# Kernel optimization log

Measured on AMD Instinct MI355X. Metric: run time of the kernel, lower is better.

## Reference

```python
import jax, jax.numpy as jnp
import numpy as np

DIM = 256; D_STATE = 16; D_CONV = 4; EXPAND = 2; NS = 64
D_INNER = EXPAND * DIM; DT_RANK = (DIM + 15) // 16
B_SZ = 2; H = 64; W = 64


def setup_inputs() -> dict:
    key = jax.random.key(0)
    ks = jax.random.split(key, 32)
    g = lambda i, shape, s=0.02: jax.random.normal(ks[i], shape, dtype=jnp.float32) * s
    inp = {}
    inp["x"] = jax.random.normal(ks[0], (B_SZ, DIM, H, W), dtype=jnp.float32)
    inp["ln_w"] = jnp.ones((DIM,), jnp.float32)
    inp["ln_b"] = jnp.zeros((DIM,), jnp.float32)
    inp["in_proj_w"] = g(1, (2 * D_INNER, DIM))
    for suf, base in (("", 2), ("_b", 10), ("_s", 18)):
        inp["conv_w" + suf] = g(base, (D_INNER, D_CONV), 0.1)
        inp["conv_b" + suf] = g(base + 1, (D_INNER,), 0.1)
        inp["x_proj_w" + suf] = g(base + 2, (DT_RANK + 2 * D_STATE, D_INNER))
        inp["dt_proj_w" + suf] = g(base + 3, (D_INNER, DT_RANK), 0.1)
        inp["dt_proj_b" + suf] = g(base + 4, (D_INNER,), 0.5)
        inp["D" + suf] = jnp.ones((D_INNER,), jnp.float32)
    A_log = jnp.tile(jnp.log(jnp.arange(1, D_STATE + 1, dtype=jnp.float32)), (D_INNER, 1))
    inp["A_log"] = A_log
    inp["A_log_b"] = A_log
    inp["A_log_s"] = A_log
    inp["out_proj_w"] = g(26, (DIM, D_INNER))
    return inp


def _silu(x):
    return x * jax.nn.sigmoid(x)


def _causal_conv(x, w, b):
    # x: (B, L, D); w: (D, K) depthwise causal conv along L
    K = w.shape[1]; L = x.shape[1]
    xp = jnp.pad(x, ((0, 0), (K - 1, 0), (0, 0)))
    y = b
    for k in range(K):
        y = y + xp[:, k:k + L, :] * w[:, k]
    return y


def _ssm_dir(x, z, conv_w, conv_b, x_proj_w, dt_proj_w, dt_proj_b, A_log, Dp):
    # one directional Mamba inner fn (no out_proj); x, z: (B, L, d_inner)
    Bsz, L, Din = x.shape
    xc = _silu(_causal_conv(x, conv_w, conv_b))
    x_dbl = xc @ x_proj_w.T  # (B, L, dt_rank + 2*d_state)
    dt_r = x_dbl[..., :DT_RANK]
    Bm = x_dbl[..., DT_RANK:DT_RANK + D_STATE]
    Cm = x_dbl[..., DT_RANK + D_STATE:]
    dt = jax.nn.softplus(dt_r @ dt_proj_w.T + dt_proj_b)  # (B, L, d_inner)
    A = -jnp.exp(A_log)  # (d_inner, d_state)

    def step(h, inp):
        dt_t, x_t, B_t, C_t = inp
        dA = jnp.exp(dt_t[..., None] * A)  # (B, d_inner, d_state)
        h = dA * h + (dt_t * x_t)[..., None] * B_t[:, None, :]
        return h, jnp.einsum('bds,bs->bd', h, C_t)

    h0 = jnp.zeros((Bsz, Din, D_STATE), x.dtype)
    _, ys = jax.lax.scan(step, h0, (dt.transpose(1, 0, 2), xc.transpose(1, 0, 2),
                                    Bm.transpose(1, 0, 2), Cm.transpose(1, 0, 2)))
    y = ys.transpose(1, 0, 2) + xc * Dp
    return y * _silu(z)


def reference(x, ln_w, ln_b, in_proj_w,
              conv_w, conv_b, x_proj_w, dt_proj_w, dt_proj_b, D,
              conv_w_b, conv_b_b, x_proj_w_b, dt_proj_w_b, dt_proj_b_b, D_b,
              conv_w_s, conv_b_s, x_proj_w_s, dt_proj_w_s, dt_proj_b_s, D_s,
              A_log, A_log_b, A_log_s, out_proj_w):
    Bsz, C, Hh, Ww = x.shape
    L = Hh * Ww
    xf = x.reshape(Bsz, C, L).transpose(0, 2, 1)  # (B, L, C)
    mu = xf.mean(-1, keepdims=True)
    var = ((xf - mu) ** 2).mean(-1, keepdims=True)
    xn = (xf - mu) / jnp.sqrt(var + 1e-5) * ln_w + ln_b
    xz = xn @ in_proj_w.T  # (B, L, 2*d_inner), shared across directions
    xin, z = xz[..., :D_INNER], xz[..., D_INNER:]
    # forward scan
    y_f = _ssm_dir(xin, z, conv_w, conv_b, x_proj_w, dt_proj_w, dt_proj_b, A_log, D)
    # backward scan (flip sequence, scan, flip back)
    y_b = _ssm_dir(xin[:, ::-1], z[:, ::-1], conv_w_b, conv_b_b, x_proj_w_b,
                   dt_proj_w_b, dt_proj_b_b, A_log_b, D_b)[:, ::-1]
    # slice-interleaved scan: 'b (s i) d -> b (i s) d' with s = NS slices
    def il(t):
        return t.reshape(Bsz, NS, L // NS, D_INNER).transpose(0, 2, 1, 3).reshape(Bsz, L, D_INNER)
    def dil(t):
        return t.reshape(Bsz, L // NS, NS, D_INNER).transpose(0, 2, 1, 3).reshape(Bsz, L, D_INNER)
    y_s = dil(_ssm_dir(il(xin), il(z), conv_w_s, conv_b_s, x_proj_w_s,
                       dt_proj_w_s, dt_proj_b_s, A_log_s, D_s))
    out = (y_f + y_b + y_s) @ out_proj_w.T  # (B, L, C)
    return x + out.transpose(0, 2, 1).reshape(Bsz, C, Hh, Ww)
```

## Files before the change

kernel.cpp:

```cpp
#include <hip/hip_runtime.h>
#include <hip/hip_bf16.h>
#include <cstdint>

#define B_SZ 2
#define DIM 256
#define L_SEQ 4096
#define D_INNER 512
#define DT_RANK 16
#define D_STATE 16
#define NCHUNK 64
#define CHUNK 64

static constexpr size_t SZ_BIG_SH = (size_t)B_SZ * L_SEQ * D_INNER;

typedef __attribute__((ext_vector_type(8))) short short8v;
typedef __attribute__((ext_vector_type(4))) short short4v;
typedef __attribute__((ext_vector_type(4))) float f32x4;

__device__ __forceinline__ float silu_f(float v) {
    return v / (1.0f + __expf(-v));
}
__device__ __forceinline__ float softplus_fast(float v) {
    return (v > 15.0f) ? v : __logf(1.0f + __expf(v));
}
__device__ __forceinline__ short f2bf(float f) {
    uint32_t u = __float_as_uint(f);
    u += 0x7fffu + ((u >> 16) & 1u);
    return (short)(u >> 16);
}
__device__ __forceinline__ float bf2f(short s) {
    return __uint_as_float(((uint32_t)(uint16_t)s) << 16);
}
__device__ __forceinline__ int dir_map(int p, int dm) {
    if (dm == 0) return p;
    if (dm == 1) return (L_SEQ - 1) - p;
    return ((p & 63) << 6) | (p >> 6);
}
__device__ __forceinline__ void pow_dA(float r1, float* dA) {
    const float r2 = r1 * r1, r4 = r2 * r2, r8 = r4 * r4;
    dA[0] = r1;         dA[1] = r2;         dA[2] = r2 * r1;    dA[3] = r4;
    dA[4] = r4 * r1;    dA[5] = r4 * r2;    dA[6] = r4 * dA[2]; dA[7] = r8;
    dA[8] = r8 * r1;    dA[9] = r8 * r2;    dA[10] = r8 * dA[2]; dA[11] = r8 * r4;
    dA[12] = r8 * dA[4]; dA[13] = r8 * dA[5]; dA[14] = r8 * dA[6]; dA[15] = r8 * r8;
}

__global__ __launch_bounds__(256) void k_cvt(
    const float* __restrict__ Wi, const float* __restrict__ Wo,
    const float* __restrict__ xp0, const float* __restrict__ xp1, const float* __restrict__ xp2,
    const float* __restrict__ dw0, const float* __restrict__ dw1, const float* __restrict__ dw2,
    short* __restrict__ Wib, short* __restrict__ Wob,
    short* __restrict__ xpwb, short* __restrict__ dtwb)
{
    const int idx = blockIdx.x * 256 + threadIdx.x;
    const float* src; short* dst; int off;
    if (idx < 65536)        { src = Wi; dst = Wib; off = idx; }
    else if (idx < 98304)   { src = Wo; dst = Wob; off = idx - 65536; }
    else if (idx < 116736)  {
        int k = idx - 98304; const int d = k / 6144; k -= d * 6144;
        src = d == 0 ? xp0 : (d == 1 ? xp1 : xp2);
        dst = xpwb + (size_t)d * 24576; off = k;
    } else {
        int k = idx - 116736; const int d = k / 2048; k -= d * 2048;
        src = d == 0 ? dw0 : (d == 1 ? dw1 : dw2);
        dst = dtwb + (size_t)d * 8192; off = k;
    }
    const float4 v = *(const float4*)(src + (size_t)off * 4);
    short4v p = {f2bf(v.x), f2bf(v.y), f2bf(v.z), f2bf(v.w)};
    *(short4v*)(dst + (size_t)off * 4) = p;
}

__global__ __launch_bounds__(256) void k_ln_t(
    const float* __restrict__ x, const float* __restrict__ lnw,
    const float* __restrict__ lnb, short* __restrict__ xnb)
{
    __shared__ float xt[64][257];
    __shared__ float red[2][4][64];
    __shared__ float muS[64], rsS[64];
    __shared__ float lnwS[DIM], lnbS[DIM];

    const int b  = blockIdx.x >> 6;
    const int l0 = (blockIdx.x & 63) << 6;
    const int t  = threadIdx.x;
    lnwS[t] = lnw[t]; lnbS[t] = lnb[t];

    const float* xb = x + (size_t)b * DIM * L_SEQ + l0;
#pragma unroll
    for (int it = 0; it < 16; ++it) {
        const int idx = it * 256 + t;
        const int c = idx >> 4, pos = (idx & 15) << 2;
        const float4 v = *(const float4*)(xb + (size_t)c * L_SEQ + pos);
        xt[pos + 0][c] = v.x; xt[pos + 1][c] = v.y;
        xt[pos + 2][c] = v.z; xt[pos + 3][c] = v.w;
    }
    __syncthreads();
    {
        const int l = t & 63, cq = t >> 6;
        float sum = 0.f, sq = 0.f;
        for (int c = cq * 64; c < cq * 64 + 64; ++c) {
            const float v = xt[l][c];
            sum += v; sq += v * v;
        }
        red[0][cq][l] = sum; red[1][cq][l] = sq;
    }
    __syncthreads();
    if (t < 64) {
        const float s  = red[0][0][t] + red[0][1][t] + red[0][2][t] + red[0][3][t];
        const float q2 = red[1][0][t] + red[1][1][t] + red[1][2][t] + red[1][3][t];
        const float mu  = s * (1.0f / DIM);
        const float var = q2 * (1.0f / DIM) - mu * mu;
        muS[t] = mu; rsS[t] = rsqrtf(var + 1e-5f);
    }
    __syncthreads();
#pragma unroll
    for (int it = 0; it < 32; ++it) {
        const int idx = it * 256 + t;
        const int l = idx >> 7, cp = (idx & 127) << 1;
        const float mu = muS[l], rs = rsS[l];
        short2 p;
        p.x = f2bf((xt[l][cp + 0] - mu) * rs * lnwS[cp + 0] + lnbS[cp + 0]);
        p.y = f2bf((xt[l][cp + 1] - mu) * rs * lnwS[cp + 1] + lnbS[cp + 1]);
        *(short2*)(xnb + (size_t)((b * L_SEQ) + l0 + l) * DIM + cp) = p;
    }
}

__global__ __launch_bounds__(256) void k_inproj_mfma(
    const short* __restrict__ xnb, const short* __restrict__ Wib,
    short* __restrict__ xinb, short* __restrict__ szb)
{
    const int mblk = blockIdx.x >> 2;
    const int q    = blockIdx.x & 3;
    const int t = threadIdx.x;
    const int w = t >> 6, l = t & 63;
    const int m0 = mblk * 64 + w * 16;
    const int n0 = q * 256;
    const int lrow = l & 15, lk = l >> 4;

    short8v a[8];
    {
        const short* ap = xnb + (size_t)(m0 + lrow) * DIM + lk * 8;
#pragma unroll
        for (int kk = 0; kk < 8; ++kk)
            a[kk] = *(const short8v*)(ap + kk * 32);
    }

#pragma unroll 4
    for (int nf = 0; nf < 16; ++nf) {
        const int n = n0 + nf * 16 + lrow;
        const short* bp = Wib + (size_t)n * DIM + lk * 8;
        f32x4 acc = {0.f, 0.f, 0.f, 0.f};
#pragma unroll
        for (int kk = 0; kk < 8; ++kk)
            acc = __builtin_amdgcn_mfma_f32_16x16x32_bf16(
                a[kk], *(const short8v*)(bp + kk * 32), acc, 0, 0, 0);
        const int col = n;
        const int r0  = m0 + lk * 4;
        if (n0 < D_INNER) {
#pragma unroll
            for (int j = 0; j < 4; ++j)
                xinb[(size_t)(r0 + j) * D_INNER + col] = f2bf(acc[j]);
        } else {
#pragma unroll
            for (int j = 0; j < 4; ++j)
                szb[(size_t)(r0 + j) * D_INNER + (col - D_INNER)] = f2bf(silu_f(acc[j]));
        }
    }
}

__global__ __launch_bounds__(256) void k_conv3(
    const short* __restrict__ xinb,
    const float* __restrict__ cw0, const float* __restrict__ cw1, const float* __restrict__ cw2,
    const float* __restrict__ cb0, const float* __restrict__ cb1, const float* __restrict__ cb2,
    short* __restrict__ xcbb, int dir_base, size_t xcb_str)
{
    const int rel = blockIdx.x >> 9;
    const int rem = blockIdx.x & 511;
    const int dir = dir_base + rel;
    const int b   = rem >> 8;
    const int p0  = (rem & 255) << 4;
    const int t   = threadIdx.x;

    const float* cw = dir == 0 ? cw0 : (dir == 1 ? cw1 : cw2);
    const float* cb = dir == 0 ? cb0 : (dir == 1 ? cb1 : cb2);
    short* xcb = xcbb + (size_t)rel * xcb_str;

    __shared__ short s[19][D_INNER];
    for (int i = 0; i < 19; ++i) {
        const int pk = p0 - 3 + i;
        short2 v = {0, 0};
        if (pk >= 0) {
            const int lo = dir_map(pk, dir);
            v = *(const short2*)(xinb + ((size_t)b * L_SEQ + lo) * D_INNER + t * 2);
        }
        *(short2*)&s[i][t * 2] = v;
    }
    __syncthreads();

#pragma unroll
    for (int half = 0; half < 2; ++half) {
        const int d = half * 256 + t;
        const float4 wv = *(const float4*)(cw + d * 4);
        const float bb = cb[d];
        float x0 = bf2f(s[0][d]), x1 = bf2f(s[1][d]), x2 = bf2f(s[2][d]);
#pragma unroll
        for (int i = 0; i < 16; ++i) {
            const float x3 = bf2f(s[i + 3][d]);
            const float a = bb + wv.x * x0 + wv.y * x1 + wv.z * x2 + wv.w * x3;
            xcb[((size_t)b * L_SEQ + p0 + i) * D_INNER + d] = f2bf(silu_f(a));
            x0 = x1; x1 = x2; x2 = x3;
        }
    }
}

__global__ __launch_bounds__(256) void k_proj3_mfma(
    const short* __restrict__ xcbb, const short* __restrict__ xpwb,
    const short* __restrict__ dtwb,
    const float* __restrict__ dtb0, const float* __restrict__ dtb1, const float* __restrict__ dtb2,
    short* __restrict__ dtYb, float* __restrict__ bcbuf,
    int dir_base, size_t xcb_str, size_t bc_str)
{
    const int rel = blockIdx.x >> 9;
    const int rem = blockIdx.x & 511;
    const int dir = dir_base + rel;
    const int m0  = rem * 16;
    const int t = threadIdx.x;
    const int w = t >> 6, l = t & 63;
    const int lrow = l & 15, lk = l >> 4;

    const short* xcb = xcbb + (size_t)rel * xcb_str;
    const short* xpw = xpwb + (size_t)dir * (48 * 512);
    const short* dtw = dtwb + (size_t)dir * (512 * 16);
    const float* dtb = dir == 0 ? dtb0 : (dir == 1 ? dtb1 : dtb2);
    short* dt = dtYb + (size_t)dir * SZ_BIG_SH;
    float* bc = bcbuf + (size_t)rel * bc_str;

    __shared__ float red[4][3][16][17];
    __shared__ short xdblb[16][16];
    __shared__ float dtbS[512];

    dtbS[t] = dtb[t]; dtbS[t + 256] = dtb[t + 256];

    short8v a[4];
    {
        const short* ap = xcb + (size_t)(m0 + lrow) * D_INNER + w * 128 + lk * 8;
#pragma unroll
        for (int kk = 0; kk < 4; ++kk)
            a[kk] = *(const short8v*)(ap + kk * 32);
    }

#pragma unroll
    for (int nf = 0; nf < 3; ++nf) {
        f32x4 acc = {0.f, 0.f, 0.f, 0.f};
        const short* bp = xpw + (size_t)(nf * 16 + lrow) * D_INNER + w * 128 + lk * 8;
#pragma unroll
        for (int kk = 0; kk < 4; ++kk)
            acc = __builtin_amdgcn_mfma_f32_16x16x32_bf16(
                a[kk], *(const short8v*)(bp + kk * 32), acc, 0, 0, 0);
#pragma unroll
        for (int j = 0; j < 4; ++j)
            red[w][nf][lk * 4 + j][lrow] = acc[j];
    }
    __syncthreads();

#pragma unroll
    for (int i = 0; i < 3; ++i) {
        const int nf = i;
        const int row = (t >> 4) & 15, col = t & 15;
        const float v = red[0][nf][row][col] + red[1][nf][row][col]
                      + red[2][nf][row][col] + red[3][nf][row][col];
        if (nf == 0) xdblb[row][col] = f2bf(v);
        else         bc[(size_t)(m0 + row) * 32 + (nf - 1) * 16 + col] = v;
    }
    __syncthreads();

    short8v adt = {0, 0, 0, 0, 0, 0, 0, 0};
    if (lk < 2) adt = *(const short8v*)&xdblb[lrow][lk * 8];

#pragma unroll
    for (int nbw = 0; nbw < 8; ++nbw) {
        const int nb = w * 8 + nbw;
        short8v bdt = {0, 0, 0, 0, 0, 0, 0, 0};
        if (lk < 2) bdt = *(const short8v*)(dtw + (size_t)(nb * 16 + lrow) * 16 + lk * 8);
        f32x4 acc = {0.f, 0.f, 0.f, 0.f};
        acc = __builtin_amdgcn_mfma_f32_16x16x32_bf16(adt, bdt, acc, 0, 0, 0);
        const int d = nb * 16 + lrow;
        const float bias = dtbS[d];
#pragma unroll
        for (int j = 0; j < 4; ++j)
            dt[(size_t)(m0 + lk * 4 + j) * D_INNER + d] = f2bf(softplus_fast(acc[j] + bias));
    }
}

template<bool FAST>
__device__ __forceinline__ void scan1_body(
    const short* dtp, const short* xcp, const float* bcp,
    short (*dts)[256], short (*xcs)[256], float (*bcs)[16],
    const float* Al_d, int t, float* Pb_o, float* Fb_o)
{
    float As20, As2[16];
    if (FAST) {
        As20 = -__expf(Al_d[0]) * 1.44269504f;
    } else {
#pragma unroll
        for (int s = 0; s < 16; ++s) As2[s] = -__expf(Al_d[s]) * 1.44269504f;
        As20 = As2[0];
    }
    float h[16];
#pragma unroll
    for (int s = 0; s < 16; ++s) h[s] = 0.f;
    float sumdt = 0.f;

    for (int tile = 0; tile < CHUNK / 16; ++tile) {
        const int p0 = tile * 16;
#pragma unroll
        for (int rep = 0; rep < 2; ++rep) {
            const int idx = rep * 256 + t;
            const int jr = idx >> 5, c8 = (idx & 31) << 3;
            *(short8v*)&dts[jr][c8] = *(const short8v*)(dtp + (size_t)(p0 + jr) * D_INNER + c8);
            *(short8v*)&xcs[jr][c8] = *(const short8v*)(xcp + (size_t)(p0 + jr) * D_INNER + c8);
        }
        if (t < 64) {
            const int jr = t >> 2, c4 = (t & 3) << 2;
            *(float4*)&bcs[jr][c4] = *(const float4*)(bcp + (size_t)(p0 + jr) * 32 + c4);
        }
        __syncthreads();

#pragma unroll
        for (int j = 0; j < 16; ++j) {
            const float dtv = bf2f(dts[j][t]);
            const float xv  = bf2f(xcs[j][t]);
            sumdt += dtv;
            const float dtx = dtv * xv;
            float Bv[16];
#pragma unroll
            for (int s4 = 0; s4 < 4; ++s4) {
                const float4 bb = *(const float4*)&bcs[j][s4 * 4];
                Bv[s4 * 4 + 0] = bb.x; Bv[s4 * 4 + 1] = bb.y;
                Bv[s4 * 4 + 2] = bb.z; Bv[s4 * 4 + 3] = bb.w;
            }
            if (FAST) {
                float dA[16];
                pow_dA(exp2f(dtv * As20), dA);
#pragma unroll
                for (int s = 0; s < 16; ++s)
                    h[s] = fmaf(dA[s], h[s], dtx * Bv[s]);
            } else {
#pragma unroll
                for (int s = 0; s < 16; ++s)
                    h[s] = fmaf(exp2f(dtv * As2[s]), h[s], dtx * Bv[s]);
            }
        }
        __syncthreads();
    }
    if (FAST) {
        float Pv[16];
        pow_dA(exp2f(sumdt * As20), Pv);
#pragma unroll
        for (int s = 0; s < 16; ++s) {
            Pb_o[(size_t)s * D_INNER] = Pv[s];
            Fb_o[(size_t)s * D_INNER] = h[s];
        }
    } else {
#pragma unroll
        for (int s = 0; s < 16; ++s) {
            Pb_o[(size_t)s * D_INNER] = exp2f(As2[s] * sumdt);
            Fb_o[(size_t)s * D_INNER] = h[s];
        }
    }
}

template<bool FAST>
__device__ __forceinline__ void scan2_body(
    short* dtp, const short* xcp, const float* bcp,
    short (*dts)[256], short (*xcs)[256], float (*bcs)[32],
    const float* Al_d, int t, float Dv, const float* Hin_o)
{
    float As20, As2[16];
    if (FAST) {
        As20 = -__expf(Al_d[0]) * 1.44269504f;
    } else {
#pragma unroll
        for (int s = 0; s < 16; ++s) As2[s] = -__expf(Al_d[s]) * 1.44269504f;
        As20 = As2[0];
    }
    float h[16];
#pragma unroll
    for (int s = 0; s < 16; ++s)
        h[s] = Hin_o[(size_t)s * D_INNER];

    for (int tile = 0; tile < CHUNK / 16; ++tile) {
        const int p0 = tile * 16;
#pragma unroll
        for (int rep = 0; rep < 2; ++rep) {
            const int idx = rep * 256 + t;
            const int jr = idx >> 5, c8 = (idx & 31) << 3;
            *(short8v*)&dts[jr][c8] = *(const short8v*)(dtp + (size_t)(p0 + jr) * D_INNER + c8);
            *(short8v*)&xcs[jr][c8] = *(const short8v*)(xcp + (size_t)(p0 + jr) * D_INNER + c8);
        }
        if (t < 128) {
            const int jr = t >> 3, c4 = (t & 7) << 2;
            *(float4*)&bcs[jr][c4] = *(const float4*)(bcp + (size_t)(p0 + jr) * 32 + c4);
        }
        __syncthreads();

#pragma unroll
        for (int j = 0; j < 16; ++j) {
            const float dtv = bf2f(dts[j][t]);
            const float xv  = bf2f(xcs[j][t]);
            const float dtx = dtv * xv;
            float Bv[16], Cv[16];
#pragma unroll
            for (int s4 = 0; s4 < 4; ++s4) {
                const float4 bb = *(const float4*)&bcs[j][s4 * 4];
                const float4 cc = *(const float4*)&bcs[j][16 + s4 * 4];
                Bv[s4 * 4 + 0] = bb.x; Bv[s4 * 4 + 1] = bb.y;
                Bv[s4 * 4 + 2] = bb.z; Bv[s4 * 4 + 3] = bb.w;
                Cv[s4 * 4 + 0] = cc.x; Cv[s4 * 4 + 1] = cc.y;
                Cv[s4 * 4 + 2] = cc.z; Cv[s4 * 4 + 3] = cc.w;
            }
            float y = xv * Dv;
            if (FAST) {
                float dA[16];
                pow_dA(exp2f(dtv * As20), dA);
#pragma unroll
                for (int s = 0; s < 16; ++s) {
                    h[s] = fmaf(dA[s], h[s], dtx * Bv[s]);
                    y = fmaf(h[s], Cv[s], y);
                }
            } else {
#pragma unroll
                for (int s = 0; s < 16; ++s) {
                    h[s] = fmaf(exp2f(dtv * As2[s]), h[s], dtx * Bv[s]);
                    y = fmaf(h[s], Cv[s], y);
                }
            }
            dtp[(size_t)(p0 + j) * D_INNER + t] = f2bf(y);
        }
        __syncthreads();
    }
}

__device__ __forceinline__ bool fast_vote(const float* Al_d, int t, int* flagS) {
    bool ok = true;
    const float a0 = __expf(Al_d[0]);
#pragma unroll
    for (int s = 1; s < 16; ++s) {
        const float v = __expf(Al_d[s]);
        const float e = (float)(s + 1) * a0;
        ok = ok && (fabsf(v - e) <= 1e-3f * e);
    }
    if (t == 0) *flagS = 1;
    __syncthreads();
    if (!ok) *flagS = 0;
    __syncthreads();
    return *flagS != 0;
}

__global__ __launch_bounds__(256, 4) void k_scan1(
    const short* __restrict__ dtYb, const short* __restrict__ xcbb,
    const float* __restrict__ bcb,
    const float* __restrict__ Al0, const float* __restrict__ Al1, const float* __restrict__ Al2,
    float* __restrict__ Pbb, float* __restrict__ Fbb,
    int dir_base, size_t xcb_str, size_t bc_str, size_t pf_str)
{
    const int rel = blockIdx.x >> 8;
    const int rem = blockIdx.x & 255;
    const int dir = dir_base + rel;
    const int b     = rem >> 7;
    const int chunk = (rem >> 1) & 63;
    const int half  = rem & 1;
    const int t = threadIdx.x;
    const int d = half * 256 + t;

    const short* dtg = dtYb + (size_t)dir * SZ_BIG_SH;
    const short* xcg = xcbb + (size_t)rel * xcb_str;
    const float* bcg = bcb + (size_t)rel * bc_str;
    const float* Al = dir == 0 ? Al0 : (dir == 1 ? Al1 : Al2);
    float* Pb = Pbb + (size_t)rel * pf_str;
    float* Fb = Fbb + (size_t)rel * pf_str;

    __shared__ short dts[16][256];
    __shared__ short xcs[16][256];
    __shared__ float bcs[16][16];
    __shared__ int flagS;

    const size_t rowbase = (size_t)b * L_SEQ + chunk * CHUNK;
    const short* dtp = dtg + rowbase * D_INNER + half * 256;
    const short* xcp = xcg + rowbase * D_INNER + half * 256;
    const float* bcp = bcg + rowbase * 32;
    const float* Al_d = Al + d * D_STATE;
    const size_t o = ((size_t)b * NCHUNK + chunk) * (D_STATE * D_INNER) + d;

    const bool fast = fast_vote(Al_d, t, &flagS);
    if (fast) scan1_body<true >(dtp, xcp, bcp, dts, xcs, bcs, Al_d, t, Pb + o, Fb + o);
    else      scan1_body<false>(dtp, xcp, bcp, dts, xcs, bcs, Al_d, t, Pb + o, Fb + o);
}

__global__ __launch_bounds__(256) void k_comb(
    float* __restrict__ PbHin, const float* __restrict__ Fbb, size_t pf_str)
{
    const int rel = blockIdx.x >> 6;
    const int gid = (blockIdx.x & 63) * 256 + threadIdx.x;
    const int b   = gid >> 13;
    const int rem = gid & 8191;
    float* PH = PbHin + (size_t)rel * pf_str;
    const float* Fb = Fbb + (size_t)rel * pf_str;
    float h = 0.f;
    for (int c = 0; c < NCHUNK; ++c) {
        const size_t i = ((size_t)(b * NCHUNK + c) << 13) + rem;
        const float pv = PH[i];
        const float fv = Fb[i];
        PH[i] = h;
        h = fv + pv * h;
    }
}

__global__ __launch_bounds__(256, 4) void k_scan2(
    short* dtYb,
    const short* __restrict__ xcbb, const float* __restrict__ bcb,
    const float* __restrict__ Al0, const float* __restrict__ Al1, const float* __restrict__ Al2,
    const float* __restrict__ Dp0, const float* __restrict__ Dp1, const float* __restrict__ Dp2,
    const float* __restrict__ Hinb,
    int dir_base, size_t xcb_str, size_t bc_str, size_t pf_str)
{
    const int rel = blockIdx.x >> 8;
    const int rem = blockIdx.x & 255;
    const int dir = dir_base + rel;
    const int b     = rem >> 7;
    const int chunk = (rem >> 1) & 63;
    const int half  = rem & 1;
    const int t = threadIdx.x;
    const int d = half * 256 + t;

    short* dtg      = dtYb + (size_t)dir * SZ_BIG_SH;
    const short* xcg = xcbb + (size_t)rel * xcb_str;
    const float* bcg = bcb + (size_t)rel * bc_str;
    const float* Al  = dir == 0 ? Al0 : (dir == 1 ? Al1 : Al2);
    const float* Dpp = dir == 0 ? Dp0 : (dir == 1 ? Dp1 : Dp2);
    const float* Hin = Hinb + (size_t)rel * pf_str;

    __shared__ short dts[16][256];
    __shared__ short xcs[16][256];
    __shared__ float bcs[16][32];
    __shared__ int flagS;

    const size_t rowbase = (size_t)b * L_SEQ + chunk * CHUNK;
    short* dtp       = dtg + rowbase * D_INNER + half * 256;
    const short* xcp = xcg + rowbase * D_INNER + half * 256;
    const float* bcp = bcg + rowbase * 32;
    const float* Al_d = Al + d * D_STATE;
    const float Dv = Dpp[d];
    const size_t o = ((size_t)b * NCHUNK + chunk) * (D_STATE * D_INNER) + d;

    const bool fast = fast_vote(Al_d, t, &flagS);
    if (fast) scan2_body<true >(dtp, xcp, bcp, dts, xcs, bcs, Al_d, t, Dv, Hin + o);
    else      scan2_body<false>(dtp, xcp, bcp, dts, xcs, bcs, Al_d, t, Dv, Hin + o);
}

__global__ __launch_bounds__(256) void k_out3_mfma(
    const short* __restrict__ yall, const short* __restrict__ szb,
    const short* __restrict__ Wob, const float* __restrict__ x,
    float* __restrict__ out)
{
    __shared__ short ytb[32][512];
    const int tile = blockIdx.x;
    const int b  = tile >> 7;
    const int l0 = (tile & 127) << 5;
    const int t  = threadIdx.x;

    const short* y0 = yall;
    const short* y1 = yall + SZ_BIG_SH;
    const short* y2 = yall + 2 * SZ_BIG_SH;
    const size_t rb = (size_t)b * L_SEQ;

#pragma unroll
    for (int it = 0; it < 8; ++it) {
        const int idx = it * 256 + t;
        const int r  = idx >> 6;
        const int c8 = idx & 63;
        const int lrow = l0 + r;
        const int p1 = (L_SEQ - 1) - lrow;
        const int p2 = ((lrow & 63) << 6) | (lrow >> 6);
        const short8v s0 = *(const short8v*)(y0 + (rb + lrow) * D_INNER + c8 * 8);
        const short8v s1 = *(const short8v*)(y1 + (rb + p1)   * D_INNER + c8 * 8);
        const short8v s2 = *(const short8v*)(y2 + (rb + p2)   * D_INNER + c8 * 8);
        const short8v sv = *(const short8v*)(szb + (rb + lrow) * D_INNER + c8 * 8);
        short8v pk;
#pragma unroll
        for (int i = 0; i < 8; ++i)
            pk[i] = f2bf((bf2f(s0[i]) + bf2f(s1[i]) + bf2f(s2[i])) * bf2f(sv[i]));
        *(short8v*)&ytb[r][(c8 ^ (r & 7)) * 8] = pk;
    }
    __syncthreads();

    const int w = t >> 6, l = t & 63;
    const int lrow = l & 15, lk = l >> 4;
    const int nf = w & 1;
    const int j0 = (w >> 1) * 128;
    const int brow = nf * 16 + lrow;

    f32x4 acc[8];
#pragma unroll
    for (int jf = 0; jf < 8; ++jf) acc[jf] = {0.f, 0.f, 0.f, 0.f};

#pragma unroll 4
    for (int kk = 0; kk < 16; ++kk) {
        const int c8 = kk * 4 + lk;
        const short8v bfrag = *(const short8v*)&ytb[brow][(c8 ^ (brow & 7)) * 8];
#pragma unroll
        for (int jf = 0; jf < 8; ++jf) {
            const short8v afrag = *(const short8v*)(
                Wob + (size_t)(j0 + jf * 16 + lrow) * D_INNER + kk * 32 + lk * 8);
            acc[jf] = __builtin_amdgcn_mfma_f32_16x16x32_bf16(afrag, bfrag, acc[jf], 0, 0, 0);
        }
    }

    const int lcol = l0 + nf * 16 + lrow;
#pragma unroll
    for (int jf = 0; jf < 8; ++jf) {
        const int jr0 = j0 + jf * 16 + lk * 4;
#pragma unroll
        for (int j = 0; j < 4; ++j) {
            const size_t o = ((size_t)b * DIM + jr0 + j) * L_SEQ + lcol;
            out[o] = x[o] + acc[jf][j];
        }
    }
}

extern "C" void kernel_launch(void* const* d_in, const int* in_sizes, int n_in,
                              void* d_out, int out_size, void* d_ws, size_t ws_size,
                              hipStream_t stream)
{
    const float* x       = (const float*)d_in[0];
    const float* ln_w    = (const float*)d_in[1];
    const float* ln_b    = (const float*)d_in[2];
    const float* in_proj = (const float*)d_in[3];
    const float* conv_w[3] = {(const float*)d_in[4],  (const float*)d_in[10], (const float*)d_in[16]};
    const float* conv_b[3] = {(const float*)d_in[5],  (const float*)d_in[11], (const float*)d_in[17]};
    const float* xpw[3]    = {(const float*)d_in[6],  (const float*)d_in[12], (const float*)d_in[18]};
    const float* dtw[3]    = {(const float*)d_in[7],  (const float*)d_in[13], (const float*)d_in[19]};
    const float* dtb[3]    = {(const float*)d_in[8],  (const float*)d_in[14], (const float*)d_in[20]};
    const float* Dp[3]     = {(const float*)d_in[9],  (const float*)d_in[15], (const float*)d_in[21]};
    const float* A_log[3]  = {(const float*)d_in[22], (const float*)d_in[23], (const float*)d_in[24]};
    const float* out_proj  = (const float*)d_in[25];
    float* out = (float*)d_out;
    (void)in_sizes; (void)n_in; (void)out_size;

    const size_t NROW   = (size_t)B_SZ * L_SEQ;
    const size_t SZ_XNB = NROW * DIM / 2;
    const size_t SZ_WIB = 262144 / 2;
    const size_t SZ_WOB = 131072 / 2;
    const size_t SZ_XPW = 3 * 24576 / 2;
    const size_t SZ_DTW = 3 * 8192 / 2;
    const size_t SZ_BH  = NROW * D_INNER / 2;
    const size_t SZ_BC  = NROW * 32;
    const size_t SZ_PF  = (size_t)B_SZ * NCHUNK * D_INNER * D_STATE;

    const size_t need_merged =
        SZ_XNB + SZ_WIB + SZ_WOB + SZ_XPW + SZ_DTW +
        2 * SZ_BH + 3 * SZ_BH + 3 * SZ_BH + 3 * SZ_BC + 6 * SZ_PF;
    const bool merged = ws_size >= need_merged * sizeof(float);
    const int ndir = merged ? 3 : 1;
    const size_t xcb_str = merged ? (SZ_BH * 2) : 0;
    const size_t bc_str  = merged ? SZ_BC : 0;
    const size_t pf_str  = merged ? SZ_PF : 0;

    float* ws   = (float*)d_ws;
    float* p    = ws;
    short* xnb  = (short*)p;  p += SZ_XNB;
    short* Wib  = (short*)p;  p += SZ_WIB;
    short* Wob  = (short*)p;  p += SZ_WOB;
    short* xpwb = (short*)p;  p += SZ_XPW;
    short* dtwb = (short*)p;  p += SZ_DTW;
    short* xinb = (short*)p;  p += SZ_BH;
    short* szb  = (short*)p;  p += SZ_BH;
    short* dtYb = (short*)p;  p += 3 * SZ_BH;
    short* xcbb = (short*)p;  p += (size_t)ndir * SZ_BH;
    float* bc   = p;          p += (size_t)ndir * SZ_BC;
    float* Pb   = p;          p += (size_t)ndir * SZ_PF;
    float* Fb   = p;          p += (size_t)ndir * SZ_PF;

    k_cvt<<<dim3(480), dim3(256), 0, stream>>>(
        in_proj, out_proj, xpw[0], xpw[1], xpw[2], dtw[0], dtw[1], dtw[2],
        Wib, Wob, xpwb, dtwb);
    k_ln_t<<<dim3(B_SZ * 64), dim3(256), 0, stream>>>(x, ln_w, ln_b, xnb);
    k_inproj_mfma<<<dim3(512), dim3(256), 0, stream>>>(xnb, Wib, xinb, szb);

    for (int d0 = 0; d0 < 3; d0 += ndir) {
        k_conv3<<<dim3(512 * ndir), dim3(256), 0, stream>>>(
            xinb, conv_w[0], conv_w[1], conv_w[2],
            conv_b[0], conv_b[1], conv_b[2], xcbb, d0, xcb_str);
        k_proj3_mfma<<<dim3(512 * ndir), dim3(256), 0, stream>>>(
            xcbb, xpwb, dtwb, dtb[0], dtb[1], dtb[2],
            dtYb, bc, d0, xcb_str, bc_str);
        k_scan1<<<dim3(256 * ndir), dim3(256), 0, stream>>>(
            dtYb, xcbb, bc, A_log[0], A_log[1], A_log[2], Pb, Fb,
            d0, xcb_str, bc_str, pf_str);
        k_comb<<<dim3(64 * ndir), dim3(256), 0, stream>>>(Pb, Fb, pf_str);
        k_scan2<<<dim3(256 * ndir), dim3(256), 0, stream>>>(
            dtYb, xcbb, bc, A_log[0], A_log[1], A_log[2],
            Dp[0], Dp[1], Dp[2], Pb, d0, xcb_str, bc_str, pf_str);
    }

    k_out3_mfma<<<dim3(256), dim3(256), 0, stream>>>(
        dtYb, szb, Wob, x, out);
}
```

Measured before the change: 237.6 us.

## Fuse chunked scan passes into single kernel with decoupled look-back

Replaces the three-kernel chunked selective scan (per-chunk partial scan, sequential chunk combine, second scan pass) with one kernel. Each block publishes its chunk's decay product and final state, then walks back through predecessor flags to assemble its incoming state, decoupled look-back style, and publishes the inclusive state for later chunks. This removes two kernel launches and the separate serial combine pass. The cost is spin-waiting on global flags, a memset per call, and a reliance on blocks being scheduled in an order that lets earlier chunks finish.

```diff
diff --git a/kernel.cpp b/kernel.cpp
--- a/kernel.cpp
+++ b/kernel.cpp
@@ -12,6 +12,7 @@
 #define CHUNK 64
 
 static constexpr size_t SZ_BIG_SH = (size_t)B_SZ * L_SEQ * D_INNER;
+static constexpr size_t PF_DIR = (size_t)B_SZ * NCHUNK * D_STATE * D_INNER;
 
 typedef __attribute__((ext_vector_type(8))) short short8v;
 typedef __attribute__((ext_vector_type(4))) short short4v;
@@ -290,11 +291,29 @@
     }
 }
 
+__device__ __forceinline__ bool fast_vote(const float* Al_d, int t, int* flagS) {
+    bool ok = true;
+    const float a0 = __expf(Al_d[0]);
+#pragma unroll
+    for (int s = 1; s < 16; ++s) {
+        const float v = __expf(Al_d[s]);
+        const float e = (float)(s + 1) * a0;
+        ok = ok && (fabsf(v - e) <= 1e-3f * e);
+    }
+    if (t == 0) *flagS = 1;
+    __syncthreads();
+    if (!ok) *flagS = 0;
+    __syncthreads();
+    return *flagS != 0;
+}
+
 template<bool FAST>
-__device__ __forceinline__ void scan1_body(
-    const short* dtp, const short* xcp, const float* bcp,
-    short (*dts)[256], short (*xcs)[256], float (*bcs)[16],
-    const float* Al_d, int t, float* Pb_o, float* Fb_o)
+__device__ __forceinline__ void scan_fused_body(
+    short* dtp, const short* xcp, const float* bcp,
+    short (*dts)[256], short (*xcs)[256], float (*bcs)[32],
+    const float* Al_d, int t, float Dv,
+    float* P, float* F, float* H,
+    int* flagBase, int b, int chunk)
 {
     float As20, As2[16];
     if (FAST) {
@@ -304,6 +323,7 @@
         for (int s = 0; s < 16; ++s) As2[s] = -__expf(Al_d[s]) * 1.44269504f;
         As20 = As2[0];
     }
+
     float h[16];
 #pragma unroll
     for (int s = 0; s < 16; ++s) h[s] = 0.f;
@@ -351,41 +371,63 @@
         }
         __syncthreads();
     }
+
+    float Pv[16];
     if (FAST) {
-        float Pv[16];
         pow_dA(exp2f(sumdt * As20), Pv);
-#pragma unroll
-        for (int s = 0; s < 16; ++s) {
-            Pb_o[(size_t)s * D_INNER] = Pv[s];
-            Fb_o[(size_t)s * D_INNER] = h[s];
-        }
     } else {
 #pragma unroll
-        for (int s = 0; s < 16; ++s) {
-            Pb_o[(size_t)s * D_INNER] = exp2f(As2[s] * sumdt);
-            Fb_o[(size_t)s * D_INNER] = h[s];
-        }
-    }
-}
-
-template<bool FAST>
-__device__ __forceinline__ void scan2_body(
-    short* dtp, const short* xcp, const float* bcp,
-    short (*dts)[256], short (*xcs)[256], float (*bcs)[32],
-    const float* Al_d, int t, float Dv, const float* Hin_o)
-{
-    float As20, As2[16];
-    if (FAST) {
-        As20 = -__expf(Al_d[0]) * 1.44269504f;
-    } else {
-#pragma unroll
-        for (int s = 0; s < 16; ++s) As2[s] = -__expf(Al_d[s]) * 1.44269504f;
-        As20 = As2[0];
-    }
-    float h[16];
+        for (int s = 0; s < 16; ++s) Pv[s] = exp2f(As2[s] * sumdt);
+    }
+
+    const size_t bbase = (size_t)b * NCHUNK * (D_STATE * D_INNER);
+    const size_t cb = bbase + (size_t)chunk * (D_STATE * D_INNER);
+#pragma unroll
+    for (int s = 0; s < 16; ++s) {
+        P[cb + (size_t)s * D_INNER] = Pv[s];
+        F[cb + (size_t)s * D_INNER] = h[s];
+    }
+    __threadfence();
+    if (t == 0)
+        __hip_atomic_store(&flagBase[chunk], 1, __ATOMIC_RELEASE, __HIP_MEMORY_SCOPE_AGENT);
+
+    float Hin[16];
+#pragma unroll
+    for (int s = 0; s < 16; ++s) Hin[s] = 0.f;
+    if (chunk > 0) {
+        float accP[16];
+#pragma unroll
+        for (int s = 0; s < 16; ++s) accP[s] = 1.f;
+        int k = chunk - 1;
+        while (true) {
+            const int st = __hip_atomic_load(&flagBase[k], __ATOMIC_ACQUIRE, __HIP_MEMORY_SCOPE_AGENT);
+            if (st == 0) { __builtin_amdgcn_s_sleep(1); continue; }
+            const size_t kb = bbase + (size_t)k * (D_STATE * D_INNER);
+            if (st == 2) {
+#pragma unroll
+                for (int s = 0; s < 16; ++s)
+                    Hin[s] = fmaf(accP[s], H[kb + (size_t)s * D_INNER], Hin[s]);
+                break;
+            } else {
+#pragma unroll
+                for (int s = 0; s < 16; ++s) {
+                    Hin[s] = fmaf(accP[s], F[kb + (size_t)s * D_INNER], Hin[s]);
+                    accP[s] *= P[kb + (size_t)s * D_INNER];
+                }
+                if (--k < 0) break;
+            }
+        }
+    }
+
 #pragma unroll
     for (int s = 0; s < 16; ++s)
-        h[s] = Hin_o[(size_t)s * D_INNER];
+        H[cb + (size_t)s * D_INNER] = fmaf(Pv[s], Hin[s], h[s]);
+    __threadfence();
+    if (t == 0)
+        __hip_atomic_store(&flagBase[chunk], 2, __ATOMIC_RELEASE, __HIP_MEMORY_SCOPE_AGENT);
+
+#pragma unroll
+    for (int s = 0; s < 16; ++s) h[s] = Hin[s];
 
     for (int tile = 0; tile < CHUNK / 16; ++tile) {
         const int p0 = tile * 16;
@@ -439,104 +481,32 @@
     }
 }
 
-__device__ __forceinline__ bool fast_vote(const float* Al_d, int t, int* flagS) {
-    bool ok = true;
-    const float a0 = __expf(Al_d[0]);
-#pragma unroll
-    for (int s = 1; s < 16; ++s) {
-        const float v = __expf(Al_d[s]);
-        const float e = (float)(s + 1) * a0;
-        ok = ok && (fabsf(v - e) <= 1e-3f * e);
-    }
-    if (t == 0) *flagS = 1;
-    __syncthreads();
-    if (!ok) *flagS = 0;
-    __syncthreads();
-    return *flagS != 0;
-}
-
-__global__ __launch_bounds__(256, 4) void k_scan1(
-    const short* __restrict__ dtYb, const short* __restrict__ xcbb,
-    const float* __restrict__ bcb,
+__global__ __launch_bounds__(256, 4) void k_scan_fused(
+    short* dtYb, const short* __restrict__ xcbb, const float* __restrict__ bcb,
     const float* __restrict__ Al0, const float* __restrict__ Al1, const float* __restrict__ Al2,
-    float* __restrict__ Pbb, float* __restrict__ Fbb,
-    int dir_base, size_t xcb_str, size_t bc_str, size_t pf_str)
+    const float* __restrict__ Dp0, const float* __restrict__ Dp1, const float* __restrict__ Dp2,
+    float* Pg, float* Fg, float* Hg, int* flags,
+    int dir_base, size_t xcb_str, size_t bc_str)
 {
     const int rel = blockIdx.x >> 8;
     const int rem = blockIdx.x & 255;
     const int dir = dir_base + rel;
+    const int chunk = rem & 63;
+    const int half  = (rem >> 6) & 1;
     const int b     = rem >> 7;
-    const int chunk = (rem >> 1) & 63;
-    const int half  = rem & 1;
     const int t = threadIdx.x;
     const int d = half * 256 + t;
 
-    const short* dtg = dtYb + (size_t)dir * SZ_BIG_SH;
-    const short* xcg = xcbb + (size_t)rel * xcb_str;
-    const float* bcg = bcb + (size_t)rel * bc_str;
-    const float* Al = dir == 0 ? Al0 : (dir == 1 ? Al1 : Al2);
-    float* Pb = Pbb + (size_t)rel * pf_str;
-    float* Fb = Fbb + (size_t)rel * pf_str;
-
-    __shared__ short dts[16][256];
-    __shared__ short xcs[16][256];
-    __shared__ float bcs[16][16];
-    __shared__ int flagS;
-
-    const size_t rowbase = (size_t)b * L_SEQ + chunk * CHUNK;
-    const short* dtp = dtg + rowbase * D_INNER + half * 256;
-    const short* xcp = xcg + rowbase * D_INNER + half * 256;
-    const float* bcp = bcg + rowbase * 32;
-    const float* Al_d = Al + d * D_STATE;
-    const size_t o = ((size_t)b * NCHUNK + chunk) * (D_STATE * D_INNER) + d;
-
-    const bool fast = fast_vote(Al_d, t, &flagS);
-    if (fast) scan1_body<true >(dtp, xcp, bcp, dts, xcs, bcs, Al_d, t, Pb + o, Fb + o);
-    else      scan1_body<false>(dtp, xcp, bcp, dts, xcs, bcs, Al_d, t, Pb + o, Fb + o);
-}
-
-__global__ __launch_bounds__(256) void k_comb(
-    float* __restrict__ PbHin, const float* __restrict__ Fbb, size_t pf_str)
-{
-    const int rel = blockIdx.x >> 6;
-    const int gid = (blockIdx.x & 63) * 256 + threadIdx.x;
-    const int b   = gid >> 13;
-    const int rem = gid & 8191;
-    float* PH = PbHin + (size_t)rel * pf_str;
-    const float* Fb = Fbb + (size_t)rel * pf_str;
-    float h = 0.f;
-    for (int c = 0; c < NCHUNK; ++c) {
-        const size_t i = ((size_t)(b * NCHUNK + c) << 13) + rem;
-        const float pv = PH[i];
-        const float fv = Fb[i];
-        PH[i] = h;
-        h = fv + pv * h;
-    }
-}
-
-__global__ __launch_bounds__(256, 4) void k_scan2(
-    short* dtYb,
-    const short* __restrict__ xcbb, const float* __restrict__ bcb,
-    const float* __restrict__ Al0, const float* __restrict__ Al1, const float* __restrict__ Al2,
-    const float* __restrict__ Dp0, const float* __restrict__ Dp1, const float* __restrict__ Dp2,
-    const float* __restrict__ Hinb,
-    int dir_base, size_t xcb_str, size_t bc_str, size_t pf_str)
-{
-    const int rel = blockIdx.x >> 8;
-    const int rem = blockIdx.x & 255;
-    const int dir = dir_base + rel;
-    const int b     = rem >> 7;
-    const int chunk = (rem >> 1) & 63;
-    const int half  = rem & 1;
-    const int t = threadIdx.x;
-    const int d = half * 256 + t;
-
-    short* dtg      = dtYb + (size_t)dir * SZ_BIG_SH;
+    short* dtg       = dtYb + (size_t)dir * SZ_BIG_SH;
     const short* xcg = xcbb + (size_t)rel * xcb_str;
     const float* bcg = bcb + (size_t)rel * bc_str;
     const float* Al  = dir == 0 ? Al0 : (dir == 1 ? Al1 : Al2);
     const float* Dpp = dir == 0 ? Dp0 : (dir == 1 ? Dp1 : Dp2);
-    const float* Hin = Hinb + (size_t)rel * pf_str;
+
+    float* P = Pg + (size_t)dir * PF_DIR + d;
+    float* F = Fg + (size_t)dir * PF_DIR + d;
+    float* H = Hg + (size_t)dir * PF_DIR + d;
+    int* flagBase = flags + ((dir * B_SZ + b) * 2 + half) * NCHUNK;
 
     __shared__ short dts[16][256];
     __shared__ short xcs[16][256];
@@ -549,11 +519,12 @@
     const float* bcp = bcg + rowbase * 32;
     const float* Al_d = Al + d * D_STATE;
     const float Dv = Dpp[d];
-    const size_t o = ((size_t)b * NCHUNK + chunk) * (D_STATE * D_INNER) + d;
 
     const bool fast = fast_vote(Al_d, t, &flagS);
-    if (fast) scan2_body<true >(dtp, xcp, bcp, dts, xcs, bcs, Al_d, t, Dv, Hin + o);
-    else      scan2_body<false>(dtp, xcp, bcp, dts, xcs, bcs, Al_d, t, Dv, Hin + o);
+    if (fast) scan_fused_body<true >(dtp, xcp, bcp, dts, xcs, bcs, Al_d, t, Dv,
+                                     P, F, H, flagBase, b, chunk);
+    else      scan_fused_body<false>(dtp, xcp, bcp, dts, xcs, bcs, Al_d, t, Dv,
+                                     P, F, H, flagBase, b, chunk);
 }
 
 __global__ __launch_bounds__(256) void k_out3_mfma(
@@ -653,16 +624,14 @@
     const size_t SZ_DTW = 3 * 8192 / 2;
     const size_t SZ_BH  = NROW * D_INNER / 2;
     const size_t SZ_BC  = NROW * 32;
-    const size_t SZ_PF  = (size_t)B_SZ * NCHUNK * D_INNER * D_STATE;
 
     const size_t need_merged =
         SZ_XNB + SZ_WIB + SZ_WOB + SZ_XPW + SZ_DTW +
-        2 * SZ_BH + 3 * SZ_BH + 3 * SZ_BH + 3 * SZ_BC + 6 * SZ_PF;
+        2 * SZ_BH + 3 * SZ_BH + 3 * SZ_BH + 3 * SZ_BC + 9 * PF_DIR + 1024;
     const bool merged = ws_size >= need_merged * sizeof(float);
     const int ndir = merged ? 3 : 1;
     const size_t xcb_str = merged ? (SZ_BH * 2) : 0;
     const size_t bc_str  = merged ? SZ_BC : 0;
-    const size_t pf_str  = merged ? SZ_PF : 0;
 
     float* ws   = (float*)d_ws;
     float* p    = ws;
@@ -676,8 +645,12 @@
     short* dtYb = (short*)p;  p += 3 * SZ_BH;
     short* xcbb = (short*)p;  p += (size_t)ndir * SZ_BH;
     float* bc   = p;          p += (size_t)ndir * SZ_BC;
-    float* Pb   = p;          p += (size_t)ndir * SZ_PF;
-    float* Fb   = p;          p += (size_t)ndir * SZ_PF;
+    float* Pg   = p;          p += 3 * PF_DIR;
+    float* Fg   = p;          p += 3 * PF_DIR;
+    float* Hg   = p;          p += 3 * PF_DIR;
+    int*   flags = (int*)p;   p += 1024;
+
+    hipMemsetAsync(flags, 0, 3 * B_SZ * 2 * NCHUNK * sizeof(int), stream);
 
     k_cvt<<<dim3(480), dim3(256), 0, stream>>>(
         in_proj, out_proj, xpw[0], xpw[1], xpw[2], dtw[0], dtw[1], dtw[2],
@@ -692,13 +665,10 @@
         k_proj3_mfma<<<dim3(512 * ndir), dim3(256), 0, stream>>>(
             xcbb, xpwb, dtwb, dtb[0], dtb[1], dtb[2],
             dtYb, bc, d0, xcb_str, bc_str);
-        k_scan1<<<dim3(256 * ndir), dim3(256), 0, stream>>>(
-            dtYb, xcbb, bc, A_log[0], A_log[1], A_log[2], Pb, Fb,
-            d0, xcb_str, bc_str, pf_str);
-        k_comb<<<dim3(64 * ndir), dim3(256), 0, stream>>>(Pb, Fb, pf_str);
-        k_scan2<<<dim3(256 * ndir), dim3(256), 0, stream>>>(
+        k_scan_fused<<<dim3(256 * ndir), dim3(256), 0, stream>>>(
             dtYb, xcbb, bc, A_log[0], A_log[1], A_log[2],
-            Dp[0], Dp[1], Dp[2], Pb, d0, xcb_str, bc_str, pf_str);
+            Dp[0], Dp[1], Dp[2], Pg, Fg, Hg, flags,
+            d0, xcb_str, bc_str);
     }
 
     k_out3_mfma<<<dim3(256), dim3(256), 0, stream>>>(
```

After: 727.8 us. 3.06x slower.
